# Kernel tuning notes

Measured on AMD Instinct MI355X. Metric: run time of the kernel, lower is better.

## Reference

```python
import jax, jax.numpy as jnp
import numpy as np

N_NODES = 50000
N_EDGES = 800000
F_IN = 128
C = 64
NODE_DEG = 32  # edges forced to touch node 0


def setup_inputs() -> dict:
    key = jax.random.key(0)
    ks = jax.random.split(key, 10)
    x = jax.random.normal(ks[0], (N_NODES, F_IN), dtype=jnp.float32)
    # random edges over nodes 1..N-1, then force the first NODE_DEG edges to have src == 0
    src = jax.random.randint(ks[1], (N_EDGES,), 1, N_NODES)
    dst = jax.random.randint(ks[2], (N_EDGES,), 1, N_NODES)
    src = src.at[:NODE_DEG].set(0)
    edge_index = jnp.stack([src, dst]).astype(jnp.int64)
    pos = jax.random.normal(ks[3], (N_NODES, 2), dtype=jnp.float32)
    batch = jnp.zeros((N_NODES,), dtype=jnp.int64)
    s1 = 1.0 / np.sqrt(F_IN)
    s2 = 1.0 / np.sqrt(C)
    w1 = jax.random.uniform(ks[4], (F_IN, C), jnp.float32, -s1, s1)
    b1 = jnp.zeros((C,), jnp.float32)
    w2 = jax.random.uniform(ks[5], (C, C), jnp.float32, -s2, s2)
    b2 = jnp.zeros((C,), jnp.float32)
    w_ro = jax.random.uniform(ks[6], (C, 1), jnp.float32, -s2, s2)
    b_ro = jnp.zeros((1,), jnp.float32)
    return {"x": x, "edge_index": edge_index, "pos": pos, "node": 0,
            "batch": batch, "w1": w1, "b1": b1, "w2": w2, "b2": b2,
            "w_ro": w_ro, "b_ro": b_ro}


def gcn_conv(x, src, dst, w, b, n_nodes):
    # PyG GCNConv: linear -> symmetric normalization with self-loops -> scatter-add
    xw = x @ w  # [N, C]
    deg = jax.ops.segment_sum(jnp.ones_like(dst, dtype=xw.dtype), dst,
                              num_segments=n_nodes) + 1.0  # +1 self-loop
    dinv = jax.lax.rsqrt(deg)
    norm = dinv[src] * dinv[dst]  # [E]
    agg = jax.ops.segment_sum(norm[:, None] * xw[src], dst, num_segments=n_nodes)
    agg = agg + xw * (dinv * dinv)[:, None]  # self-loop contribution
    return agg + b


def reference(x, edge_index, pos, node, batch, w1, b1, w2, b2, w_ro, b_ro):
    n_nodes = x.shape[0]
    src, dst = edge_index[0], edge_index[1]
    h = jax.nn.relu(gcn_conv(x, src, dst, w1, b1, n_nodes))
    h = jax.nn.relu(gcn_conv(h, src, dst, w2, b2, n_nodes))
    # select edges incident to `node` (data-dependent size; eager boolean indexing)
    mask = (src == node) | (dst == node)
    rel = edge_index[:, mask]  # [2, K]
    targets = jnp.where(rel[0] == node, rel[1], rel[0])  # [K]
    score = jax.nn.sigmoid(h[targets] @ w_ro + b_ro)  # [K, 1]
    return score[:, 0], targets
```

## Files before the change

### kernel.cpp

```cpp
#include <hip/hip_runtime.h>
#include <math.h>

#define F_IN 128
#define C 64
#define ELCAP 128
#define E2CAP 4096
#define E1CAP 32768
#define S1CAP 4096
#define NBW 1568
#define SCAP 512
#define NSCAN 256

#define I_EL 0
#define I_E2 1
#define I_E1 2
#define I_S1 3

__global__ __launch_bounds__(256) void mask_hist_kernel(const int* __restrict__ src,
    const int* __restrict__ dst, const int* __restrict__ node_p,
    int* __restrict__ deg, unsigned* __restrict__ tbits, unsigned* __restrict__ s1bits,
    int* __restrict__ map1, int* __restrict__ elist, int* __restrict__ s1list,
    int* __restrict__ e1s, int* __restrict__ e1d, int* __restrict__ cnt, int nq) {
  int q = blockIdx.x * 256 + threadIdx.x;
  if (q >= nq) return;
  int node = *node_p;
  int4 s4 = ((const int4*)src)[q];
  int4 d4 = ((const int4*)dst)[q];
  int ss[4] = {s4.x, s4.y, s4.z, s4.w};
  int dd[4] = {d4.x, d4.y, d4.z, d4.w};
#pragma unroll
  for (int j = 0; j < 4; ++j) {
    int s = ss[j], d = dd[j];
    atomicAdd(&deg[d], 1);
    if (s == node || d == node) {
      int p = atomicAdd(&cnt[I_EL], 1);
      if (p < ELCAP) elist[p] = q * 4 + j;
      int tgt = (s == node) ? d : s;
      atomicOr(&tbits[tgt >> 5], 1u << (tgt & 31));
      unsigned old = atomicOr(&s1bits[tgt >> 5], 1u << (tgt & 31));
      if (!((old >> (tgt & 31)) & 1)) {
        int idx = atomicAdd(&cnt[I_S1], 1);
        if (idx < S1CAP) { s1list[idx] = tgt; map1[tgt] = idx; }
        int pe = atomicAdd(&cnt[I_E1], 1);
        if (pe < E1CAP) { e1s[pe] = tgt; e1d[pe] = tgt; }
      }
    }
  }
}

__global__ __launch_bounds__(256) void scanB_kernel(const int* __restrict__ src,
    const int* __restrict__ dst, const unsigned* __restrict__ tbits,
    unsigned* __restrict__ s1bits, int* __restrict__ map1, int* __restrict__ s1list,
    int* __restrict__ e2s, int* __restrict__ e2d, int* __restrict__ e1s,
    int* __restrict__ e1d, int* __restrict__ cnt, int nq) {
  __shared__ unsigned tb[NBW];
  __shared__ int ebS[SCAP], ebD[SCAP], nb[SCAP];
  __shared__ int cA, cB, bA, bB, bC;
  int t = threadIdx.x;
  for (int i = t; i < NBW; i += 256) tb[i] = tbits[i];
  if (t == 0) { cA = 0; cB = 0; }
  __syncthreads();
  const int4* s4p = (const int4*)src;
  const int4* d4p = (const int4*)dst;
  for (int q = blockIdx.x * 256 + t; q < nq; q += gridDim.x * 256) {
    int4 d4 = d4p[q];
    int4 s4 = s4p[q];
    int dd[4] = {d4.x, d4.y, d4.z, d4.w};
    int ss[4] = {s4.x, s4.y, s4.z, s4.w};
#pragma unroll
    for (int j = 0; j < 4; ++j) {
      int d = dd[j];
      if ((tb[d >> 5] >> (d & 31)) & 1) {
        int s = ss[j];
        int p = atomicAdd(&cA, 1);
        if (p < SCAP) { ebS[p] = s; ebD[p] = d; }
        else { int g = atomicAdd(&cnt[I_E2], 1); if (g < E2CAP) { e2s[g] = s; e2d[g] = d; } }
        unsigned old = atomicOr(&s1bits[s >> 5], 1u << (s & 31));
        if (!((old >> (s & 31)) & 1)) {
          int p2 = atomicAdd(&cB, 1);
          if (p2 < SCAP) nb[p2] = s;
          else {
            int idx = atomicAdd(&cnt[I_S1], 1);
            if (idx < S1CAP) { s1list[idx] = s; map1[s] = idx; }
            int pe = atomicAdd(&cnt[I_E1], 1);
            if (pe < E1CAP) { e1s[pe] = s; e1d[pe] = s; }
          }
        }
      }
    }
  }
  __syncthreads();
  int nA = min(cA, SCAP), nB = min(cB, SCAP);
  if (t == 0) {
    bA = atomicAdd(&cnt[I_E2], nA);
    bB = atomicAdd(&cnt[I_S1], nB);
    bC = atomicAdd(&cnt[I_E1], nB);
  }
  __syncthreads();
  for (int i = t; i < nA; i += 256) {
    int g = bA + i; if (g < E2CAP) { e2s[g] = ebS[i]; e2d[g] = ebD[i]; }
  }
  for (int i = t; i < nB; i += 256) {
    int v = nb[i];
    int idx = bB + i; if (idx < S1CAP) { s1list[idx] = v; map1[v] = idx; }
    int pe = bC + i; if (pe < E1CAP) { e1s[pe] = v; e1d[pe] = v; }
  }
}

__global__ __launch_bounds__(256) void scanC_kernel(const int* __restrict__ src,
    const int* __restrict__ dst, const unsigned* __restrict__ s1bits,
    int* __restrict__ e1s, int* __restrict__ e1d, int* __restrict__ cnt, int nq) {
  __shared__ unsigned sb[NBW];
  __shared__ int ebS[SCAP], ebD[SCAP];
  __shared__ int cA, bA;
  int t = threadIdx.x;
  for (int i = t; i < NBW; i += 256) sb[i] = s1bits[i];
  if (t == 0) cA = 0;
  __syncthreads();
  const int4* s4p = (const int4*)src;
  const int4* d4p = (const int4*)dst;
  for (int q = blockIdx.x * 256 + t; q < nq; q += gridDim.x * 256) {
    int4 d4 = d4p[q];
    int4 s4 = s4p[q];
    int dd[4] = {d4.x, d4.y, d4.z, d4.w};
    int ss[4] = {s4.x, s4.y, s4.z, s4.w};
#pragma unroll
    for (int j = 0; j < 4; ++j) {
      int d = dd[j];
      if ((sb[d >> 5] >> (d & 31)) & 1) {
        int s = ss[j];
        int p = atomicAdd(&cA, 1);
        if (p < SCAP) { ebS[p] = s; ebD[p] = d; }
        else { int g = atomicAdd(&cnt[I_E1], 1); if (g < E1CAP) { e1s[g] = s; e1d[g] = d; } }
      }
    }
  }
  __syncthreads();
  int nA = min(cA, SCAP);
  if (t == 0) bA = atomicAdd(&cnt[I_E1], nA);
  __syncthreads();
  for (int i = t; i < nA; i += 256) {
    int g = bA + i; if (g < E1CAP) { e1s[g] = ebS[i]; e1d[g] = ebD[i]; }
  }
}

__global__ __launch_bounds__(256) void edgegemm1_kernel(const float* __restrict__ x,
    const float* __restrict__ w, const int* __restrict__ e1s,
    const int* __restrict__ e1d, const int* __restrict__ deg,
    const int* __restrict__ map1, float* __restrict__ agg1c,
    const int* __restrict__ cnt) {
  __shared__ float ws[F_IN * C];
  __shared__ float xs[32 * F_IN];
  __shared__ int qidx[32];
  __shared__ float wgt[32];
  int t = threadIdx.x;
  int n1 = cnt[I_E1]; if (n1 > E1CAP) n1 = E1CAP;
  int s1c = cnt[I_S1]; if (s1c > S1CAP) s1c = S1CAP;
  int ntile = (n1 + 31) / 32;
  if ((int)blockIdx.x >= ntile) return;
  for (int i = t; i < F_IN * C; i += 256) ws[i] = w[i];
  for (int tile = blockIdx.x; tile < ntile; tile += gridDim.x) {
    __syncthreads();
    int r0 = tile * 32;
    for (int i = t; i < 32 * F_IN; i += 256) {
      int r = r0 + (i >> 7);
      xs[i] = (r < n1) ? x[(size_t)e1s[r] * F_IN + (i & 127)] : 0.0f;
    }
    if (t < 32) {
      int r = r0 + t;
      if (r < n1) {
        int s = e1s[r], d = e1d[r];
        int q = map1[d];
        qidx[t] = ((unsigned)q < (unsigned)s1c) ? q : -1;
        wgt[t] = rsqrtf((float)deg[s] + 1.0f) * rsqrtf((float)deg[d] + 1.0f);
      } else qidx[t] = -1;
    }
    __syncthreads();
    int c = t & 63, rb = t >> 6;
    float acc[8];
#pragma unroll
    for (int j = 0; j < 8; ++j) acc[j] = 0.f;
    for (int k = 0; k < F_IN; ++k) {
      float wv = ws[k * C + c];
#pragma unroll
      for (int j = 0; j < 8; ++j)
        acc[j] += xs[(rb + j * 4) * F_IN + k] * wv;
    }
#pragma unroll
    for (int j = 0; j < 8; ++j) {
      int r = rb + j * 4;
      int q = qidx[r];
      if (q >= 0) atomicAdd(&agg1c[(size_t)q * C + c], acc[j] * wgt[r]);
    }
  }
}

__global__ __launch_bounds__(256) void gemm2c_kernel(const float* __restrict__ agg1c,
    const float* __restrict__ b1, const float* __restrict__ w,
    float* __restrict__ xw2c, const int* __restrict__ cnt) {
  __shared__ float ws[C * C];
  __shared__ float xs[64 * C];
  int t = threadIdx.x;
  int sc = cnt[I_S1]; if (sc > S1CAP) sc = S1CAP;
  for (int i = t; i < C * C; i += 256) ws[i] = w[i];
  int ntile = (sc + 63) / 64;
  for (int tile = blockIdx.x; tile < ntile; tile += gridDim.x) {
    __syncthreads();
    int r0 = tile * 64;
    for (int i = t; i < 64 * C; i += 256) {
      int r = r0 + (i >> 6), cc = i & 63;
      xs[i] = (r < sc) ? fmaxf(agg1c[(size_t)r * C + cc] + b1[cc], 0.0f) : 0.0f;
    }
    __syncthreads();
    int c = t & 63, rb = t >> 6;
    float acc[16];
#pragma unroll
    for (int j = 0; j < 16; ++j) acc[j] = 0.f;
    for (int k = 0; k < C; ++k) {
      float wv = ws[k * C + c];
#pragma unroll
      for (int j = 0; j < 16; ++j)
        acc[j] += xs[(rb + j * 4) * C + k] * wv;
    }
#pragma unroll
    for (int j = 0; j < 16; ++j) {
      int r = r0 + rb + j * 4;
      if (r < sc) xw2c[(size_t)r * C + c] = acc[j];
    }
  }
}

__global__ __launch_bounds__(256) void gather2_kernel(const int* __restrict__ e2s,
    const int* __restrict__ e2d, const int* __restrict__ deg,
    const int* __restrict__ map1, const float* __restrict__ xw2c,
    float* __restrict__ agg2c, const int* __restrict__ cnt) {
  int n2 = cnt[I_E2]; if (n2 > E2CAP) n2 = E2CAP;
  int gid = blockIdx.x * 256 + threadIdx.x;
  int i = gid >> 6, lane = gid & 63;
  int stride = (gridDim.x * 256) >> 6;
  for (; i < n2; i += stride) {
    int s = e2s[i], d = e2d[i];
    int q = map1[d];
    if ((unsigned)q < (unsigned)ELCAP) {
      float w = rsqrtf((float)deg[s] + 1.0f) * rsqrtf((float)deg[d] + 1.0f);
      atomicAdd(&agg2c[(size_t)q * C + lane], w * xw2c[(size_t)map1[s] * C + lane]);
    }
  }
}

__global__ __launch_bounds__(1024) void readout_kernel(const int* __restrict__ src,
    const int* __restrict__ dst, const float* __restrict__ agg2c,
    const int* __restrict__ deg, const int* __restrict__ map1,
    const float* __restrict__ xw2c, const float* __restrict__ b2,
    const float* __restrict__ w_ro, const float* __restrict__ b_ro,
    const int* __restrict__ node_p, const int* __restrict__ elist,
    const int* __restrict__ cnt, int K, float* __restrict__ out) {
  __shared__ int ids[ELCAP];
  __shared__ float wro_s[C], b2_s[C];
  int t = threadIdx.x;
  int n = cnt[I_EL];
  if (n > K) n = K;
  if (n > ELCAP) n = ELCAP;
  if (t < C) { wro_s[t] = w_ro[t]; b2_s[t] = b2[t]; }
  for (int i = t; i < n; i += 1024) ids[i] = elist[i];
  __syncthreads();
  int node = *node_p;
  float bro = b_ro[0];
  int wid = t >> 6, lane = t & 63;
  for (int i = wid; i < n; i += 16) {
    int eid = ids[i];
    int rank = 0;
    for (int j = 0; j < n; ++j) rank += (ids[j] < eid) ? 1 : 0;
    int s = src[eid], d = dst[eid];
    int tgt = (s == node) ? d : s;
    int q = map1[tgt];
    float dv = rsqrtf((float)deg[tgt] + 1.0f);
    float h = agg2c[(size_t)q * C + lane] + xw2c[(size_t)q * C + lane] * dv * dv
            + b2_s[lane];
    float v = fmaxf(h, 0.0f) * wro_s[lane];
#pragma unroll
    for (int off = 1; off < 64; off <<= 1) v += __shfl_xor(v, off, 64);
    if (lane == 0) {
      float acc = v + bro;
      out[rank] = 1.0f / (1.0f + expf(-acc));
      out[K + rank] = (float)tgt;
    }
  }
}

extern "C" void kernel_launch(void* const* d_in, const int* in_sizes, int n_in,
                              void* d_out, int out_size, void* d_ws, size_t ws_size,
                              hipStream_t stream) {
  const float* x    = (const float*)d_in[0];
  const int*   ei   = (const int*)d_in[1];
  const int*   node = (const int*)d_in[3];
  const float* w1   = (const float*)d_in[5];
  const float* b1   = (const float*)d_in[6];
  const float* w2   = (const float*)d_in[7];
  const float* b2   = (const float*)d_in[8];
  const float* w_ro = (const float*)d_in[9];
  const float* b_ro = (const float*)d_in[10];
  float* out = (float*)d_out;

  int nE = in_sizes[1] / 2;
  int nN = in_sizes[0] / F_IN;
  const int* src = ei;
  const int* dst = ei + nE;
  int K = out_size / 2;
  int nq = nE / 4;

  int* w = (int*)d_ws;
  int*      deg    = w;            w += nN;
  unsigned* tbits  = (unsigned*)w; w += NBW;
  unsigned* s1bits = (unsigned*)w; w += NBW;
  int*      cnt    = w;            w += 16;
  float*    agg1c  = (float*)w;    w += (size_t)S1CAP * C;
  float*    agg2c  = (float*)w;    w += (size_t)ELCAP * C;
  int*      map1   = w;            w += nN;
  int*      elist  = w;            w += ELCAP;
  int*      s1list = w;            w += S1CAP;
  int*      e2s    = w;            w += E2CAP;
  int*      e2d    = w;            w += E2CAP;
  int*      e1s    = w;            w += E1CAP;
  int*      e1d    = w;            w += E1CAP;
  float*    xw2c   = (float*)w;    w += (size_t)S1CAP * C;

  hipMemsetAsync(deg, 0,
      ((size_t)nN + 2 * NBW + 16 + (size_t)S1CAP * C + (size_t)ELCAP * C) * 4, stream);

  mask_hist_kernel<<<(nq + 255) / 256, 256, 0, stream>>>(src, dst, node, deg, tbits,
      s1bits, map1, elist, s1list, e1s, e1d, cnt, nq);
  scanB_kernel<<<NSCAN, 256, 0, stream>>>(src, dst, tbits, s1bits, map1, s1list,
      e2s, e2d, e1s, e1d, cnt, nq);
  scanC_kernel<<<NSCAN, 256, 0, stream>>>(src, dst, s1bits, e1s, e1d, cnt, nq);
  edgegemm1_kernel<<<512, 256, 0, stream>>>(x, w1, e1s, e1d, deg, map1, agg1c, cnt);
  gemm2c_kernel<<<16, 256, 0, stream>>>(agg1c, b1, w2, xw2c, cnt);
  gather2_kernel<<<64, 256, 0, stream>>>(e2s, e2d, deg, map1, xw2c, agg2c, cnt);
  readout_kernel<<<1, 1024, 0, stream>>>(src, dst, agg2c, deg, map1, xw2c, b2,
                                         w_ro, b_ro, node, elist, cnt, K, out);
}
```

Measured before the change: 106.6 us.

## Compute degrees only for nodes in the receptive field instead of all nodes

Removes the global per-edge degree atomicAdd from the mask pass. Instead, scanC records the source nodes of 2-hop edges in a new bitset, and a new deg_kernel rescans dst and counts only edges whose destination lies in the union of the 1-hop and source bitsets. This avoids 800K scattered global atomics but adds an extra pass over dst and another kernel launch. It assumes degrees are only read for nodes in those sets.

```diff
diff --git a/kernel.cpp b/kernel.cpp
--- a/kernel.cpp
+++ b/kernel.cpp
@@ -16,9 +16,9 @@
 #define I_E1 2
 #define I_S1 3
 
-__global__ __launch_bounds__(256) void mask_hist_kernel(const int* __restrict__ src,
+__global__ __launch_bounds__(256) void mask_kernel(const int* __restrict__ src,
     const int* __restrict__ dst, const int* __restrict__ node_p,
-    int* __restrict__ deg, unsigned* __restrict__ tbits, unsigned* __restrict__ s1bits,
+    unsigned* __restrict__ tbits, unsigned* __restrict__ s1bits,
     int* __restrict__ map1, int* __restrict__ elist, int* __restrict__ s1list,
     int* __restrict__ e1s, int* __restrict__ e1d, int* __restrict__ cnt, int nq) {
   int q = blockIdx.x * 256 + threadIdx.x;
@@ -31,7 +31,6 @@
 #pragma unroll
   for (int j = 0; j < 4; ++j) {
     int s = ss[j], d = dd[j];
-    atomicAdd(&deg[d], 1);
     if (s == node || d == node) {
       int p = atomicAdd(&cnt[I_EL], 1);
       if (p < ELCAP) elist[p] = q * 4 + j;
@@ -109,7 +108,8 @@
 
 __global__ __launch_bounds__(256) void scanC_kernel(const int* __restrict__ src,
     const int* __restrict__ dst, const unsigned* __restrict__ s1bits,
-    int* __restrict__ e1s, int* __restrict__ e1d, int* __restrict__ cnt, int nq) {
+    unsigned* __restrict__ s0bits, int* __restrict__ e1s, int* __restrict__ e1d,
+    int* __restrict__ cnt, int nq) {
   __shared__ unsigned sb[NBW];
   __shared__ int ebS[SCAP], ebD[SCAP];
   __shared__ int cA, bA;
@@ -129,6 +129,7 @@
       int d = dd[j];
       if ((sb[d >> 5] >> (d & 31)) & 1) {
         int s = ss[j];
+        atomicOr(&s0bits[s >> 5], 1u << (s & 31));
         int p = atomicAdd(&cA, 1);
         if (p < SCAP) { ebS[p] = s; ebD[p] = d; }
         else { int g = atomicAdd(&cnt[I_E1], 1); if (g < E1CAP) { e1s[g] = s; e1d[g] = d; } }
@@ -141,6 +142,25 @@
   __syncthreads();
   for (int i = t; i < nA; i += 256) {
     int g = bA + i; if (g < E1CAP) { e1s[g] = ebS[i]; e1d[g] = ebD[i]; }
+  }
+}
+
+__global__ __launch_bounds__(256) void deg_kernel(const int* __restrict__ dst,
+    const unsigned* __restrict__ s0bits, const unsigned* __restrict__ s1bits,
+    int* __restrict__ deg, int nq) {
+  __shared__ unsigned cb[NBW];
+  int t = threadIdx.x;
+  for (int i = t; i < NBW; i += 256) cb[i] = s0bits[i] | s1bits[i];
+  __syncthreads();
+  const int4* d4p = (const int4*)dst;
+  for (int q = blockIdx.x * 256 + t; q < nq; q += gridDim.x * 256) {
+    int4 d4 = d4p[q];
+    int dd[4] = {d4.x, d4.y, d4.z, d4.w};
+#pragma unroll
+    for (int j = 0; j < 4; ++j) {
+      int d = dd[j];
+      if ((cb[d >> 5] >> (d & 31)) & 1) atomicAdd(&deg[d], 1);
+    }
   }
 }
 
@@ -313,6 +333,7 @@
   int*      deg    = w;            w += nN;
   unsigned* tbits  = (unsigned*)w; w += NBW;
   unsigned* s1bits = (unsigned*)w; w += NBW;
+  unsigned* s0bits = (unsigned*)w; w += NBW;
   int*      cnt    = w;            w += 16;
   float*    agg1c  = (float*)w;    w += (size_t)S1CAP * C;
   float*    agg2c  = (float*)w;    w += (size_t)ELCAP * C;
@@ -326,13 +347,14 @@
   float*    xw2c   = (float*)w;    w += (size_t)S1CAP * C;
 
   hipMemsetAsync(deg, 0,
-      ((size_t)nN + 2 * NBW + 16 + (size_t)S1CAP * C + (size_t)ELCAP * C) * 4, stream);
-
-  mask_hist_kernel<<<(nq + 255) / 256, 256, 0, stream>>>(src, dst, node, deg, tbits,
-      s1bits, map1, elist, s1list, e1s, e1d, cnt, nq);
+      ((size_t)nN + 3 * NBW + 16 + (size_t)S1CAP * C + (size_t)ELCAP * C) * 4, stream);
+
+  mask_kernel<<<(nq + 255) / 256, 256, 0, stream>>>(src, dst, node, tbits, s1bits,
+      map1, elist, s1list, e1s, e1d, cnt, nq);
   scanB_kernel<<<NSCAN, 256, 0, stream>>>(src, dst, tbits, s1bits, map1, s1list,
       e2s, e2d, e1s, e1d, cnt, nq);
-  scanC_kernel<<<NSCAN, 256, 0, stream>>>(src, dst, s1bits, e1s, e1d, cnt, nq);
+  scanC_kernel<<<NSCAN, 256, 0, stream>>>(src, dst, s1bits, s0bits, e1s, e1d, cnt, nq);
+  deg_kernel<<<NSCAN, 256, 0, stream>>>(dst, s0bits, s1bits, deg, nq);
   edgegemm1_kernel<<<512, 256, 0, stream>>>(x, w1, e1s, e1d, deg, map1, agg1c, cnt);
   gemm2c_kernel<<<16, 256, 0, stream>>>(agg1c, b1, w2, xw2c, cnt);
   gather2_kernel<<<64, 256, 0, stream>>>(e2s, e2d, deg, map1, xw2c, agg2c, cnt);
```

After: 88.00 us. 1.21x faster.
